# Kernel tuning notes

Measured on AMD Instinct MI355X. Metric: run time of the kernel, lower is better.

The kernel has to match this reference:

```python
import jax, jax.numpy as jnp
import numpy as np


def setup_inputs() -> dict:
    key = jax.random.key(0)
    k1, k2, k3 = jax.random.split(key, 3)
    N, C, H, W, K = 4, 128, 40, 30, 64
    return {
        "x": jax.random.normal(k1, (N, C, H, W), dtype=jnp.float32),
        "conv_w": jax.random.normal(k2, (K, C), dtype=jnp.float32) * 0.1,  # 1x1 conv weight [K,C,1,1] squeezed
        "centroids": jax.random.uniform(k3, (K, C), dtype=jnp.float32),
        "patch_size": 5,
        "stride": 1,
    }


def reference(x, conv_w, centroids, patch_size, stride):
    N, C, H, W = x.shape
    K = centroids.shape[0]
    # descriptor-wise L2 normalization (torch F.normalize semantics, eps=1e-12)
    norm = jnp.sqrt(jnp.sum(x * x, axis=1, keepdims=True))
    xn = x / jnp.maximum(norm, 1e-12)
    # 1x1 conv (no bias) + softmax over clusters -> soft assignment [N,K,H,W]
    logits = jnp.einsum('nchw,kc->nkhw', xn, conv_w)
    sa = jax.nn.softmax(logits, axis=1)
    # residuals [N,K,C,H,W]: (x - c_k) * a_k, then flatten K,C
    res = (xn[:, None, :, :, :] - centroids[None, :, :, None, None]) * sa[:, :, None, :, :]
    res = res.reshape(N, K * C, H, W)
    # 2D integral image with top-left zero padding -> [N,KC,H+1,W+1]
    I = jnp.cumsum(jnp.cumsum(res, axis=-1), axis=-2)
    I = jnp.pad(I, ((0, 0), (0, 0), (1, 0), (1, 0)))
    # box-filter via integral-image differencing (equivalent to the grouped
    # dilated 2x2 conv with weights [[+1,-1],[-1,+1]], stride=s, dilation=p)
    p, s = int(patch_size), int(stride)
    out = (I[:, :, p::s, p::s] - I[:, :, p::s, :-p:s]
           - I[:, :, :-p:s, p::s] + I[:, :, :-p:s, :-p:s])
    return out / (p * p)
```

## Files before the change

### kernel.cpp

```cpp
#include <hip/hip_runtime.h>

#define C_ 128
#define K_ 64
#define H_ 40
#define W_ 30
#define N_ 4
#define HW_ 1200
#define P_ 5
#define OH_ 36
#define OW_ 26
#define OHW_ 936

template<int CTRL>
__device__ __forceinline__ float dpp0f(float v) {
  return __int_as_float(__builtin_amdgcn_update_dpp(
      0, __float_as_int(v), CTRL, 0xF, 0xF, true));
}
__device__ __forceinline__ float swz_x16(float v) {
  return __int_as_float(__builtin_amdgcn_ds_swizzle(__float_as_int(v), 0x401F));
}

__global__ __launch_bounds__(256) void k1_prep(
    const float* __restrict__ x, const float* __restrict__ cw,
    float* __restrict__ xn, float* __restrict__ sa)
{
  __shared__ float xs[C_][8];
  __shared__ float wt[C_][66];
  __shared__ float part[32][8];
  __shared__ float ls[K_][9];
  __shared__ float rnorm_s[8];

  const int tid = threadIdx.x;
  const int bid = blockIdx.x;
  const int n   = bid / 150;
  const int rem = (bid - n*150) * 8;

  for (int e = tid; e < C_*K_; e += 256) {
    const int c = e >> 6, kk = e & 63;
    wt[c][kk] = cw[kk*C_ + c];
  }
  for (int e = tid; e < C_*8; e += 256) {
    const int c = e >> 3, p2 = e & 7;
    xs[c][p2] = x[((size_t)n*C_ + c)*HW_ + rem + p2];
  }
  __syncthreads();

  const int pl = tid & 7;
  const int kq = tid >> 3;
  {
    float s = 0.f;
    #pragma unroll
    for (int cc = 0; cc < 4; ++cc) {
      const float v = xs[kq*4 + cc][pl];
      s = fmaf(v, v, s);
    }
    part[kq][pl] = s;
  }
  __syncthreads();
  if (tid < 8) {
    float s = 0.f;
    #pragma unroll
    for (int q = 0; q < 32; ++q) s += part[q][tid];
    rnorm_s[tid] = 1.f / fmaxf(sqrtf(s), 1e-12f);
  }
  __syncthreads();

  {
    float a0 = 0.f, a1 = 0.f;
    #pragma unroll 8
    for (int c = 0; c < C_; ++c) {
      const float xv = xs[c][pl];
      const float2 w2 = *(const float2*)&wt[c][kq*2];
      a0 = fmaf(xv, w2.x, a0);
      a1 = fmaf(xv, w2.y, a1);
    }
    const float rn = rnorm_s[pl];
    ls[kq*2 + 0][pl] = a0 * rn;
    ls[kq*2 + 1][pl] = a1 * rn;
  }
  for (int e = tid; e < C_*8; e += 256) {
    const int c = e >> 3, p2 = e & 7;
    xn[((size_t)n*C_ + c)*HW_ + rem + p2] = xs[c][p2] * rnorm_s[p2];
  }
  __syncthreads();

  const int lane = tid & 63;
  const int wv   = tid >> 6;
  #pragma unroll
  for (int r = 0; r < 2; ++r) {
    const int p = wv + (r << 2);
    const float v = ls[lane][p];
    float mx = v;
    #pragma unroll
    for (int m = 1; m < 64; m <<= 1) mx = fmaxf(mx, __shfl_xor(mx, m, 64));
    const float e = expf(v - mx);
    float s = e;
    #pragma unroll
    for (int m = 1; m < 64; m <<= 1) s += __shfl_xor(s, m, 64);
    sa[((size_t)n*K_ + lane)*HW_ + rem + p] = e / s;
  }
}

__global__ __launch_bounds__(256) void k2_box(
    const float* __restrict__ xn, const float* __restrict__ sa,
    const float* __restrict__ cent, float* __restrict__ out)
{
  const int tid = threadIdx.x;
  const int w   = tid & 31;
  const int wc  = (w < W_) ? w : (W_ - 1);
  const int c   = (blockIdx.x << 3) + (tid >> 5);
  const int k   = blockIdx.y;
  const int n   = blockIdx.z;

  const float cv = cent[k*C_ + c];
  const float* __restrict__ xp = xn + (size_t)(n*C_ + c)*HW_ + wc;
  const float* __restrict__ sp = sa + (size_t)(n*K_ + k)*HW_ + wc;

  float q[H_];
  #pragma unroll
  for (int h = 0; h < H_; ++h) {
    q[h] = (xp[h*W_] - cv) * sp[h*W_];
  }

  float vq = q[0] + q[1] + q[2] + q[3] + q[4];
  float* __restrict__ op = out + (size_t)((n*K_ + k)*C_ + c)*OHW_ + w;

  #pragma unroll
  for (int i = 0; i < OH_; ++i) {
    const float sw = swz_x16(vq);
    float hs = vq;
    hs += dpp0f<0x101>(vq) + dpp0f<0x11F>(sw);
    hs += dpp0f<0x102>(vq) + dpp0f<0x11E>(sw);
    hs += dpp0f<0x103>(vq) + dpp0f<0x11D>(sw);
    hs += dpp0f<0x104>(vq) + dpp0f<0x11C>(sw);
    if (w < OW_) op[i*OW_] = hs * (1.f / (P_*P_));
    if (i < OH_ - 1) vq += q[i + P_] - q[i];
  }
}

extern "C" void kernel_launch(void* const* d_in, const int* in_sizes, int n_in,
                              void* d_out, int out_size, void* d_ws, size_t ws_size,
                              hipStream_t stream) {
  const float* x  = (const float*)d_in[0];
  const float* cw = (const float*)d_in[1];
  const float* ce = (const float*)d_in[2];

  float* xn = (float*)d_ws;
  float* sa = xn + (size_t)N_*C_*HW_;
  float* out = (float*)d_out;

  k1_prep<<<dim3(600), dim3(256), 0, stream>>>(x, cw, xn, sa);
  k2_box<<<dim3(C_/8, K_, N_), dim3(256), 0, stream>>>(xn, sa, ce, out);
}
```

Baseline: 51.21 us.

## Vectorize prep kernel and split box kernel rows across two blocks

The prep kernel now loads x with float4 into a pixel-major transposed tile and reads conv weights straight from global memory as float4 instead of staging a transposed copy in LDS. It also restructures the norm and softmax reductions to use block-wide LDS partials plus small shuffles, with vectorized stores. The box kernel splits each image's output rows into two halves of 18, doubling the grid and cutting the per-thread register array from 40 to 22. It also adds an occupancy hint of 6 blocks per SM. The split recomputes overlapping input rows (22 of 40 per half) in exchange for more parallelism and lower register pressure.

```diff
diff --git a/kernel.cpp b/kernel.cpp
--- a/kernel.cpp
+++ b/kernel.cpp
@@ -20,88 +20,121 @@
   return __int_as_float(__builtin_amdgcn_ds_swizzle(__float_as_int(v), 0x401F));
 }
 
-__global__ __launch_bounds__(256) void k1_prep(
+__global__ __launch_bounds__(256) void k1_fused(
     const float* __restrict__ x, const float* __restrict__ cw,
     float* __restrict__ xn, float* __restrict__ sa)
 {
-  __shared__ float xs[C_][8];
-  __shared__ float wt[C_][66];
-  __shared__ float part[32][8];
-  __shared__ float ls[K_][9];
+  __shared__ float xs[8][132];
+  __shared__ float ls[8][68];
+  __shared__ float red[8][36];
   __shared__ float rnorm_s[8];
+  __shared__ float smax_s[8];
+  __shared__ float rsum_s[8];
 
   const int tid = threadIdx.x;
   const int bid = blockIdx.x;
   const int n   = bid / 150;
   const int rem = (bid - n*150) * 8;
+  const float* __restrict__ xb = x + (size_t)n*C_*HW_ + rem;
 
-  for (int e = tid; e < C_*K_; e += 256) {
-    const int c = e >> 6, kk = e & 63;
-    wt[c][kk] = cw[kk*C_ + c];
-  }
-  for (int e = tid; e < C_*8; e += 256) {
-    const int c = e >> 3, p2 = e & 7;
-    xs[c][p2] = x[((size_t)n*C_ + c)*HW_ + rem + p2];
+  {
+    const int c  = tid >> 1;
+    const int p0 = (tid & 1) << 2;
+    const float4 v = *(const float4*)(xb + (size_t)c*HW_ + p0);
+    xs[p0+0][c] = v.x; xs[p0+1][c] = v.y;
+    xs[p0+2][c] = v.z; xs[p0+3][c] = v.w;
   }
   __syncthreads();
 
-  const int pl = tid & 7;
-  const int kq = tid >> 3;
+  const int pix = tid & 7;
+  const int q   = tid >> 3;
+
   {
-    float s = 0.f;
-    #pragma unroll
-    for (int cc = 0; cc < 4; ++cc) {
-      const float v = xs[kq*4 + cc][pl];
-      s = fmaf(v, v, s);
-    }
-    part[kq][pl] = s;
+    const float4 v = *(const float4*)&xs[pix][q*4];
+    red[pix][q] = (v.x*v.x + v.y*v.y) + (v.z*v.z + v.w*v.w);
   }
   __syncthreads();
-  if (tid < 8) {
-    float s = 0.f;
-    #pragma unroll
-    for (int q = 0; q < 32; ++q) s += part[q][tid];
-    rnorm_s[tid] = 1.f / fmaxf(sqrtf(s), 1e-12f);
+  if (tid < 64) {
+    const int p = tid >> 3, j = tid & 7;
+    float s = ((red[p][j] + red[p][j+8]) + (red[p][j+16] + red[p][j+24]));
+    s += __shfl_xor(s, 1, 64); s += __shfl_xor(s, 2, 64); s += __shfl_xor(s, 4, 64);
+    if (j == 0) rnorm_s[p] = 1.f / fmaxf(sqrtf(s), 1e-12f);
   }
   __syncthreads();
 
   {
+    const float* __restrict__ w0 = cw + (q*2)*C_;
+    const float* __restrict__ w1 = w0 + C_;
     float a0 = 0.f, a1 = 0.f;
     #pragma unroll 8
-    for (int c = 0; c < C_; ++c) {
-      const float xv = xs[c][pl];
-      const float2 w2 = *(const float2*)&wt[c][kq*2];
-      a0 = fmaf(xv, w2.x, a0);
-      a1 = fmaf(xv, w2.y, a1);
+    for (int c0 = 0; c0 < C_; c0 += 4) {
+      const float4 xv = *(const float4*)&xs[pix][c0];
+      const float4 wa = *(const float4*)(w0 + c0);
+      const float4 wb = *(const float4*)(w1 + c0);
+      a0 = fmaf(wa.x, xv.x, a0); a0 = fmaf(wa.y, xv.y, a0);
+      a0 = fmaf(wa.z, xv.z, a0); a0 = fmaf(wa.w, xv.w, a0);
+      a1 = fmaf(wb.x, xv.x, a1); a1 = fmaf(wb.y, xv.y, a1);
+      a1 = fmaf(wb.z, xv.z, a1); a1 = fmaf(wb.w, xv.w, a1);
     }
-    const float rn = rnorm_s[pl];
-    ls[kq*2 + 0][pl] = a0 * rn;
-    ls[kq*2 + 1][pl] = a1 * rn;
+    const float rn = rnorm_s[pix];
+    float2 lv; lv.x = a0 * rn; lv.y = a1 * rn;
+    *(float2*)&ls[pix][q*2] = lv;
   }
-  for (int e = tid; e < C_*8; e += 256) {
-    const int c = e >> 3, p2 = e & 7;
-    xn[((size_t)n*C_ + c)*HW_ + rem + p2] = xs[c][p2] * rnorm_s[p2];
+
+  {
+    const int c  = tid >> 1;
+    const int p0 = (tid & 1) << 2;
+    float4 o;
+    o.x = xs[p0+0][c] * rnorm_s[p0+0];
+    o.y = xs[p0+1][c] * rnorm_s[p0+1];
+    o.z = xs[p0+2][c] * rnorm_s[p0+2];
+    o.w = xs[p0+3][c] * rnorm_s[p0+3];
+    *(float4*)(xn + ((size_t)n*C_ + c)*HW_ + rem + p0) = o;
   }
   __syncthreads();
 
-  const int lane = tid & 63;
-  const int wv   = tid >> 6;
-  #pragma unroll
-  for (int r = 0; r < 2; ++r) {
-    const int p = wv + (r << 2);
-    const float v = ls[lane][p];
-    float mx = v;
-    #pragma unroll
-    for (int m = 1; m < 64; m <<= 1) mx = fmaxf(mx, __shfl_xor(mx, m, 64));
-    const float e = expf(v - mx);
-    float s = e;
-    #pragma unroll
-    for (int m = 1; m < 64; m <<= 1) s += __shfl_xor(s, m, 64);
-    sa[((size_t)n*K_ + lane)*HW_ + rem + p] = e / s;
+  if (tid < 64) {
+    const int p = tid >> 3, j = tid & 7;
+    const float4 v0 = *(const float4*)&ls[p][j*8];
+    const float4 v1 = *(const float4*)&ls[p][j*8 + 4];
+    float m = fmaxf(fmaxf(fmaxf(v0.x, v0.y), fmaxf(v0.z, v0.w)),
+                    fmaxf(fmaxf(v1.x, v1.y), fmaxf(v1.z, v1.w)));
+    m = fmaxf(m, __shfl_xor(m, 1, 64));
+    m = fmaxf(m, __shfl_xor(m, 2, 64));
+    m = fmaxf(m, __shfl_xor(m, 4, 64));
+    if (j == 0) smax_s[p] = m;
+  }
+  __syncthreads();
+
+  {
+    const float m = smax_s[pix];
+    const float2 lv = *(const float2*)&ls[pix][q*2];
+    const float e0 = expf(lv.x - m);
+    const float e1 = expf(lv.y - m);
+    float2 ev; ev.x = e0; ev.y = e1;
+    *(float2*)&ls[pix][q*2] = ev;
+    red[pix][q] = e0 + e1;
+  }
+  __syncthreads();
+  if (tid < 64) {
+    const int p = tid >> 3, j = tid & 7;
+    float s = ((red[p][j] + red[p][j+8]) + (red[p][j+16] + red[p][j+24]));
+    s += __shfl_xor(s, 1, 64); s += __shfl_xor(s, 2, 64); s += __shfl_xor(s, 4, 64);
+    if (j == 0) rsum_s[p] = 1.f / s;
+  }
+  __syncthreads();
+
+  {
+    const int k  = tid >> 2;
+    const int ph = (tid & 3) << 1;
+    float2 o;
+    o.x = ls[ph + 0][k] * rsum_s[ph + 0];
+    o.y = ls[ph + 1][k] * rsum_s[ph + 1];
+    *(float2*)(sa + ((size_t)n*K_ + k)*HW_ + rem + ph) = o;
   }
 }
 
-__global__ __launch_bounds__(256) void k2_box(
+__global__ __launch_bounds__(256, 6) void k2_box(
     const float* __restrict__ xn, const float* __restrict__ sa,
     const float* __restrict__ cent, float* __restrict__ out)
 {
@@ -110,23 +143,26 @@
   const int wc  = (w < W_) ? w : (W_ - 1);
   const int c   = (blockIdx.x << 3) + (tid >> 5);
   const int k   = blockIdx.y;
-  const int n   = blockIdx.z;
+  const int nh  = blockIdx.z;
+  const int n   = nh >> 1;
+  const int r0  = (nh & 1) * 18;
 
   const float cv = cent[k*C_ + c];
-  const float* __restrict__ xp = xn + (size_t)(n*C_ + c)*HW_ + wc;
-  const float* __restrict__ sp = sa + (size_t)(n*K_ + k)*HW_ + wc;
+  const float* __restrict__ xp = xn + (size_t)(n*C_ + c)*HW_ + (size_t)r0*W_ + wc;
+  const float* __restrict__ sp = sa + (size_t)(n*K_ + k)*HW_ + (size_t)r0*W_ + wc;
 
-  float q[H_];
+  float q[22];
   #pragma unroll
-  for (int h = 0; h < H_; ++h) {
+  for (int h = 0; h < 22; ++h) {
     q[h] = (xp[h*W_] - cv) * sp[h*W_];
   }
 
   float vq = q[0] + q[1] + q[2] + q[3] + q[4];
-  float* __restrict__ op = out + (size_t)((n*K_ + k)*C_ + c)*OHW_ + w;
+  float* __restrict__ op = out + (size_t)((n*K_ + k)*C_ + c)*OHW_
+                               + (size_t)r0*OW_ + w;
 
   #pragma unroll
-  for (int i = 0; i < OH_; ++i) {
+  for (int i = 0; i < 18; ++i) {
     const float sw = swz_x16(vq);
     float hs = vq;
     hs += dpp0f<0x101>(vq) + dpp0f<0x11F>(sw);
@@ -134,7 +170,7 @@
     hs += dpp0f<0x103>(vq) + dpp0f<0x11D>(sw);
     hs += dpp0f<0x104>(vq) + dpp0f<0x11C>(sw);
     if (w < OW_) op[i*OW_] = hs * (1.f / (P_*P_));
-    if (i < OH_ - 1) vq += q[i + P_] - q[i];
+    if (i < 17) vq += q[i + P_] - q[i];
   }
 }
 
@@ -149,6 +185,6 @@
   float* sa = xn + (size_t)N_*C_*HW_;
   float* out = (float*)d_out;
 
-  k1_prep<<<dim3(600), dim3(256), 0, stream>>>(x, cw, xn, sa);
-  k2_box<<<dim3(C_/8, K_, N_), dim3(256), 0, stream>>>(xn, sa, ce, out);
+  k1_fused<<<dim3(600), dim3(256), 0, stream>>>(x, cw, xn, sa);
+  k2_box  <<<dim3(C_/8, K_, N_*2), dim3(256), 0, stream>>>(xn, sa, ce, out);
 }
```

Measured after the change: 42.35 us. 17.3% less time.
